# Kernel tuning notes

Measured on AMD Instinct MI355X. Metric: run time of the kernel, lower is better.

Reference implementation:

```python
import jax, jax.numpy as jnp
import numpy as np
from jax import lax

B, H, W = 32, 80, 80
K = 100                        # max_candidates
THRESH = 0.1                   # minutiae_threshold
DIST_T = 16.0
ANGLE_T = np.pi / 6.0
PI = np.pi


def _gauss_kernel1d(ks, sigma):
    c = jnp.arange(ks, dtype=jnp.float32) - ks // 2
    g = jnp.exp(-(c * c) / (2.0 * sigma * sigma))
    return g / g.sum()


def _gaussian_blur(img):  # [B,1,H,W], separable 5x5 sigma=1.5
    k = _gauss_kernel1d(5, 1.5)
    dn = ('NCHW', 'OIHW', 'NCHW')
    x = lax.conv_general_dilated(img, k.reshape(1, 1, 1, 5), (1, 1), [(0, 0), (2, 2)], dimension_numbers=dn)
    x = lax.conv_general_dilated(x, k.reshape(1, 1, 5, 1), (1, 1), [(2, 2), (0, 0)], dimension_numbers=dn)
    return x


def _up8(m):  # nearest-neighbor x8 upsample on last two dims
    return jnp.repeat(jnp.repeat(m, 8, axis=-2), 8, axis=-1)


def _detect_and_nms(score, ori, xoff, yoff):
    # score [H,W]; ori [90,H,W]; xoff/yoff [8,H,W]
    vals, idx = lax.top_k(score.reshape(-1), K)   # sorted descending == argsort by score
    valid = vals > THRESH
    rows = idx // W
    cols = idx % W
    ang_idx = jnp.argmax(ori[:, rows, cols], axis=0)   # [K]
    xo = jnp.argmax(xoff[:, rows, cols], axis=0)
    yo = jnp.argmax(yoff[:, rows, cols], axis=0)
    angles = (ang_idx.astype(jnp.float32) * 2.0 - 89.0) * (PI / 180.0)
    x = cols.astype(jnp.float32) * 8.0 + xo.astype(jnp.float32)
    y = rows.astype(jnp.float32) * 8.0 + yo.astype(jnp.float32)
    mnt = jnp.stack([x, y, angles, vals], axis=-1)     # [K,4]
    # pairwise suppression mask (cdist + circular angle delta)
    d2 = jnp.sum((mnt[:, None, :2] - mnt[None, :, :2]) ** 2, axis=-1)
    dist = jnp.sqrt(d2)
    ad = jnp.abs(angles[:, None] - angles[None, :])
    am = jnp.minimum(ad, 2.0 * PI - ad)
    sup = (dist < DIST_T) & (am < ANGLE_T)
    ar = jnp.arange(K)
    def body(i, keep):
        s = sup[i] & (ar > i)
        return jnp.where(keep[i], keep & ~s, keep)
    keep = lax.fori_loop(0, K, body, valid)
    return mnt, keep


def setup_inputs() -> dict:
    key = jax.random.key(0)
    ks = jax.random.split(key, 7)
    return {
        'segmentation': jax.random.uniform(ks[0], (B, 1, H, W), jnp.float32),
        'minutiae_score': jax.random.uniform(ks[1], (B, 1, H, W), jnp.float32),
        'minutiae_orientation': jax.random.normal(ks[2], (B, 90, H, W), jnp.float32),
        'minutiae_x_offset': jax.random.normal(ks[3], (B, 8, H, W), jnp.float32),
        'minutiae_y_offset': jax.random.normal(ks[4], (B, 8, H, W), jnp.float32),
        'orientation': jax.random.normal(ks[5], (B, 90, H, W), jnp.float32),
        'enhanced_real': jax.random.normal(ks[6], (B, 1, 8 * H, 8 * W), jnp.float32),
    }


def reference(segmentation, minutiae_score, minutiae_orientation,
              minutiae_x_offset, minutiae_y_offset, orientation, enhanced_real):
    # --- segmentation mask: round -> gaussian blur -> round
    cleaned = jnp.round(_gaussian_blur(jnp.round(segmentation[:, 0])[:, None]))[:, 0]  # [B,H,W]
    cleaned_up = _up8(cleaned)                                                          # [B,8H,8W]
    # --- minutiae detection (threshold via masked top-k) + sequential NMS
    score = minutiae_score[:, 0] * cleaned
    mnt, keep = jax.vmap(_detect_and_nms)(score, minutiae_orientation,
                                          minutiae_x_offset, minutiae_y_offset)
    # --- orientation field
    ori_idx = jnp.argmax(orientation, axis=1).astype(jnp.float32)   # [B,H,W]
    ori_field = (_up8(ori_idx) * 2.0 - 89.0) * (PI / 180.0) * cleaned_up
    # --- enhanced image: mask + per-image min-max normalize to [0,255]
    enh = enhanced_real[:, 0] * cleaned_up
    ef = enh.reshape(B, -1)
    emin = jnp.min(ef, axis=1, keepdims=True)
    emax = jnp.max(ef, axis=1, keepdims=True)
    enorm = (ef - emin) / (emax - emin + 1e-8)
    enh_visual = enorm.reshape(B, 8 * H, 8 * W) * 255.0
    return (mnt, keep.astype(jnp.float32), enh_visual, cleaned_up * 255.0, ori_field)
```

## Files before the change

### kernel.cpp

```cpp
#include <hip/hip_runtime.h>
#include <math.h>

#define BN  32
#define H   80
#define W   80
#define HW  6400
#define KC  100
#define NCH 90
#define UW  640
#define UHW 409600

static constexpr size_t OUT_MNT   = 0;
static constexpr size_t OUT_KEEP  = (size_t)BN * KC * 4;
static constexpr size_t OUT_ENH   = OUT_KEEP + (size_t)BN * KC;
static constexpr size_t OUT_CLEAN = OUT_ENH + (size_t)BN * UHW;
static constexpr size_t OUT_ORI   = OUT_CLEAN + (size_t)BN * UHW;

#define PI_F 3.14159265358979323846
#define MM_BLOCKS 64
#define ORI_MEGA  400
#define CAP 2048
#define GAT_BLOCKS 800
#define FIN_BLOCKS 12800

typedef float vfloat4 __attribute__((ext_vector_type(4)));

__device__ __forceinline__ unsigned enc_f(float f) {
    unsigned u = __float_as_uint(f);
    return (u & 0x80000000u) ? ~u : (u | 0x80000000u);
}
__device__ __forceinline__ float dec_f(unsigned k) {
    return (k & 0x80000000u) ? __uint_as_float(k ^ 0x80000000u) : __uint_as_float(~k);
}
__device__ __forceinline__ unsigned long long shflx(unsigned long long v, int off) {
    unsigned hi = (unsigned)__shfl_xor((int)(unsigned)(v >> 32), off);
    unsigned lo = (unsigned)__shfl_xor((int)(unsigned)(v & 0xffffffffull), off);
    return ((unsigned long long)hi << 32) | lo;
}

__global__ __launch_bounds__(512) void k_clean(const float* __restrict__ seg,
                                               float* __restrict__ cleaned_g) {
    __shared__ float s_in[12 * 80];
    __shared__ float s_h[12 * 80];
    const int blk = blockIdx.x;
    const int b = blk / 10, band = blk % 10;
    const int r0 = band * 8 - 2;
    const int tid = threadIdx.x;

    float g[5];
    {
        float s = 0.f;
        #pragma unroll
        for (int i = 0; i < 5; i++) {
            float c = (float)(i - 2);
            g[i] = expf(-(c * c) / 4.5f);
            s += g[i];
        }
        #pragma unroll
        for (int i = 0; i < 5; i++) g[i] /= s;
    }

    for (int i = tid; i < 12 * 80; i += 512) {
        int lr = i / 80, w = i % 80;
        int gr = r0 + lr;
        s_in[i] = (gr >= 0 && gr < H) ? rintf(seg[(size_t)b * HW + gr * W + w]) : 0.f;
    }
    __syncthreads();
    for (int i = tid; i < 12 * 80; i += 512) {
        int lr = i / 80, w = i % 80;
        float acc = 0.f;
        #pragma unroll
        for (int dx = -2; dx <= 2; dx++) {
            int ww = w + dx;
            if (ww >= 0 && ww < W) acc += s_in[lr * 80 + ww] * g[dx + 2];
        }
        s_h[i] = acc;
    }
    __syncthreads();
    for (int i = tid; i < 8 * 80; i += 512) {
        int k = i / 80, w = i % 80;
        float acc = 0.f;
        #pragma unroll
        for (int dy = 0; dy < 5; dy++) acc += s_h[(k + dy) * 80 + w] * g[dy];
        cleaned_g[(size_t)b * HW + (band * 8 + k) * W + w] = rintf(acc);
    }
}

__global__ __launch_bounds__(512) void k_mega(const float* __restrict__ mscore,
                                              const float* __restrict__ cleaned,
                                              const float* __restrict__ ori,
                                              const float* __restrict__ enh,
                                              float* __restrict__ ori_idx,
                                              float* __restrict__ pmin,
                                              float* __restrict__ pmax,
                                              int* __restrict__ ws_idx,
                                              float* __restrict__ ws_val) {
    __shared__ __align__(16) char um[20480];
    __shared__ unsigned long long s_sel[KC];
    __shared__ unsigned s_rm[HW / 32];
    __shared__ int s_cnt[5];
    __shared__ int s_n;
    __shared__ float s_T;
    __shared__ int s_mode;
    __shared__ float smin[8], smax[8];

    const int bx = blockIdx.x, tid = threadIdx.x;
    const int lane = tid & 63;

    if (bx < BN) {
        unsigned long long* s_cand = (unsigned long long*)um;
        unsigned long long* s_red  = (unsigned long long*)um + CAP;
        const int b = bx;

        if (tid < HW / 32) s_rm[tid] = 0u;
        if (tid < 5) s_cnt[tid] = 0;
        __syncthreads();

        float sc[13];
        #pragma unroll
        for (int j = 0; j < 13; j++) {
            int i = j * 512 + tid;
            sc[j] = (i < HW) ? mscore[(size_t)b * HW + i] * cleaned[(size_t)b * HW + i]
                             : -1.0f;
        }

        int c0 = 0, c1 = 0, c2 = 0, c3 = 0, c4 = 0;
        #pragma unroll
        for (int j = 0; j < 13; j++) {
            float v = sc[j];
            c0 += (v > 0.95f); c1 += (v > 0.9f); c2 += (v > 0.8f);
            c3 += (v > 0.5f);  c4 += (v > 0.0f);
        }
        #pragma unroll
        for (int off = 32; off > 0; off >>= 1) {
            c0 += __shfl_xor(c0, off); c1 += __shfl_xor(c1, off);
            c2 += __shfl_xor(c2, off); c3 += __shfl_xor(c3, off);
            c4 += __shfl_xor(c4, off);
        }
        if (lane == 0) {
            atomicAdd(&s_cnt[0], c0); atomicAdd(&s_cnt[1], c1);
            atomicAdd(&s_cnt[2], c2); atomicAdd(&s_cnt[3], c3);
            atomicAdd(&s_cnt[4], c4);
        }
        __syncthreads();

        if (tid == 0) {
            int n95 = s_cnt[0], n90 = s_cnt[1], n80 = s_cnt[2], n50 = s_cnt[3], n0 = s_cnt[4];
            int mode; float T = 0.f;
            if (n0 < KC)                      { mode = 1; }
            else if (n95 >= KC && n95 <= CAP) { mode = 0; T = 0.95f; }
            else if (n90 >= KC && n90 <= CAP) { mode = 0; T = 0.9f; }
            else if (n80 >= KC && n80 <= CAP) { mode = 0; T = 0.8f; }
            else if (n50 >= KC && n50 <= CAP) { mode = 0; T = 0.5f; }
            else if (n0 <= CAP)               { mode = 0; T = 0.0f; }
            else                              { mode = 2; }
            s_mode = mode; s_T = T; s_n = 0;
        }
        __syncthreads();
        const int mode = s_mode;

        if (mode != 2) {
            const float T = s_T;
            #pragma unroll
            for (int j = 0; j < 13; j++) {
                int i = j * 512 + tid;
                bool take = (mode == 0) ? (sc[j] > T)
                                        : (sc[j] > 0.f || (i < 256 && sc[j] == 0.0f));
                if (take) {
                    int pos = atomicAdd(&s_n, 1);
                    s_cand[pos] = ((unsigned long long)enc_f(sc[j]) << 32) | (unsigned)(HW - i);
                }
            }
            __syncthreads();
            const int n = s_n;
            for (int c = tid; c < n; c += 512) {
                unsigned long long kk = s_cand[c];
                int rank = 0;
                for (int m = 0; m < n; m++) rank += (s_cand[m] > kk) ? 1 : 0;
                if (rank < KC) s_sel[rank] = kk;
            }
            __syncthreads();
        } else {
            for (int k = 0; k < KC; k++) {
                unsigned long long lmax = 0ull;
                #pragma unroll
                for (int j = 0; j < 13; j++) {
                    int i = j * 512 + tid;
                    if (i < HW && sc[j] >= 0.f && !((s_rm[i >> 5] >> (i & 31)) & 1u)) {
                        unsigned long long kk =
                            ((unsigned long long)enc_f(sc[j]) << 32) | (unsigned)(HW - i);
                        if (kk > lmax) lmax = kk;
                    }
                }
                s_red[tid] = lmax;
                __syncthreads();
                for (int off = 256; off > 0; off >>= 1) {
                    if (tid < off) {
                        unsigned long long o = s_red[tid + off];
                        if (o > s_red[tid]) s_red[tid] = o;
                    }
                    __syncthreads();
                }
                if (tid == 0) {
                    unsigned long long wkey = s_red[0];
                    s_sel[k] = wkey;
                    int wi = HW - (int)(wkey & 0xffffffffull);
                    s_rm[wi >> 5] |= 1u << (wi & 31);
                }
                __syncthreads();
            }
        }

        if (tid < KC) {
            unsigned long long e = s_sel[tid];
            ws_idx[(size_t)b * KC + tid] = HW - (int)(e & 0xffffffffull);
            ws_val[(size_t)b * KC + tid] = dec_f((unsigned)(e >> 32));
        }
    } else if (bx < BN + ORI_MEGA) {
        float4* s_bv = (float4*)um;
        float4* s_bj = (float4*)um + 512;
        const int grp = tid >> 7, ln = tid & 127;
        const int p4 = (bx - BN) * 128 + ln;
        const int b = p4 / (HW / 4), pp = p4 % (HW / 4);
        const float4* o = (const float4*)(ori + (size_t)b * NCH * HW) + pp;
        const int cs = (grp * NCH) >> 2, ce = ((grp + 1) * NCH) >> 2;

        float4 bv = o[(size_t)cs * (HW / 4)];
        float4 bj = make_float4((float)cs, (float)cs, (float)cs, (float)cs);
        for (int j = cs + 1; j < ce; j++) {
            float4 v = o[(size_t)j * (HW / 4)];
            if (v.x > bv.x) { bv.x = v.x; bj.x = (float)j; }
            if (v.y > bv.y) { bv.y = v.y; bj.y = (float)j; }
            if (v.z > bv.z) { bv.z = v.z; bj.z = (float)j; }
            if (v.w > bv.w) { bv.w = v.w; bj.w = (float)j; }
        }
        s_bv[tid] = bv; s_bj[tid] = bj;
        __syncthreads();
        if (grp == 0) {
            #pragma unroll
            for (int g = 1; g < 4; g++) {
                float4 v = s_bv[g * 128 + ln], jx = s_bj[g * 128 + ln];
                if (v.x > bv.x) { bv.x = v.x; bj.x = jx.x; }
                if (v.y > bv.y) { bv.y = v.y; bj.y = jx.y; }
                if (v.z > bv.z) { bv.z = v.z; bj.z = jx.z; }
                if (v.w > bv.w) { bv.w = v.w; bj.w = jx.w; }
            }
            ((float4*)ori_idx)[p4] = bj;
        }
    } else {
        const int mb = bx - (BN + ORI_MEGA);
        const int b = mb >> 6, chunk = mb & 63;
        const float4* e4 = (const float4*)(enh + (size_t)b * UHW);
        const float* cb = cleaned + (size_t)b * HW;

        float vmin = INFINITY, vmax = -INFINITY;
        for (int i = chunk * 512 + tid; i < UHW / 4; i += MM_BLOCKS * 512) {
            float4 v = e4[i];
            int p = i * 4;
            int Y = p / UW, X = p % UW;
            float c = cb[(Y >> 3) * W + (X >> 3)];
            float a = v.x * c, bb = v.y * c, cc = v.z * c, dd = v.w * c;
            vmin = fminf(vmin, fminf(fminf(a, bb), fminf(cc, dd)));
            vmax = fmaxf(vmax, fmaxf(fmaxf(a, bb), fmaxf(cc, dd)));
        }
        #pragma unroll
        for (int off = 32; off > 0; off >>= 1) {
            vmin = fminf(vmin, __shfl_xor(vmin, off));
            vmax = fmaxf(vmax, __shfl_xor(vmax, off));
        }
        int wave = tid >> 6;
        if (lane == 0) { smin[wave] = vmin; smax[wave] = vmax; }
        __syncthreads();
        if (tid == 0) {
            float m0 = smin[0], m1 = smax[0];
            #pragma unroll
            for (int wv = 1; wv < 8; wv++) {
                m0 = fminf(m0, smin[wv]);
                m1 = fmaxf(m1, smax[wv]);
            }
            pmin[b * MM_BLOCKS + chunk] = m0;
            pmax[b * MM_BLOCKS + chunk] = m1;
        }
    }
}

__global__ __launch_bounds__(256) void k_fg(const float* __restrict__ enh,
                                            const float* __restrict__ cleaned,
                                            const float* __restrict__ ori_idx,
                                            const float* __restrict__ pmin,
                                            const float* __restrict__ pmax,
                                            const float* __restrict__ mori,
                                            const float* __restrict__ mxo,
                                            const float* __restrict__ myo,
                                            const int* __restrict__ ws_idx,
                                            const float* __restrict__ ws_val,
                                            float* __restrict__ out) {
    const int bx = blockIdx.x, tid = threadIdx.x;

    if (bx < GAT_BLOCKS) {
        const int lane = tid & 63;
        const int wid = bx * 4 + (tid >> 6);
        const int b = wid / KC, k = wid % KC;
        const int idx = ws_idx[(size_t)b * KC + k];

        const float* pm = mori + (size_t)b * NCH * HW + idx;
        unsigned long long kk =
            ((unsigned long long)enc_f(pm[(size_t)lane * HW]) << 32) | (unsigned)(127 - lane);
        if (lane < NCH - 64) {
            unsigned long long k1 =
                ((unsigned long long)enc_f(pm[(size_t)(64 + lane) * HW]) << 32)
                | (unsigned)(127 - (64 + lane));
            if (k1 > kk) kk = k1;
        }
        unsigned long long kx = 0ull, ky = 0ull;
        if (lane >= 32 && lane < 40)
            kx = ((unsigned long long)enc_f(mxo[((size_t)b * 8 + (lane - 32)) * HW + idx]) << 32)
                 | (unsigned)(15 - (lane - 32));
        if (lane >= 40 && lane < 48)
            ky = ((unsigned long long)enc_f(myo[((size_t)b * 8 + (lane - 40)) * HW + idx]) << 32)
                 | (unsigned)(15 - (lane - 40));

        #pragma unroll
        for (int off = 32; off > 0; off >>= 1) {
            unsigned long long o;
            o = shflx(kk, off); if (o > kk) kk = o;
            o = shflx(kx, off); if (o > kx) kx = o;
            o = shflx(ky, off); if (o > ky) ky = o;
        }

        if (lane == 0) {
            int ch = 127 - (int)(kk & 0xffffffffull);
            int xo = 15  - (int)(kx & 0xffffffffull);
            int yo = 15  - (int)(ky & 0xffffffffull);
            int r = idx / W, c = idx % W;
            float4 m;
            m.x = (float)c * 8.0f + (float)xo;
            m.y = (float)r * 8.0f + (float)yo;
            m.z = ((float)ch * 2.0f - 89.0f) * (float)(PI_F / 180.0);
            m.w = ws_val[(size_t)b * KC + k];
            ((float4*)(out + OUT_MNT))[(size_t)b * KC + k] = m;
        }
    } else {
        __shared__ float s_emin, s_emax;
        const int fb = bx - GAT_BLOCKS;
        const int b = fb / 400;
        if (tid < 64) {
            float vmin = pmin[b * MM_BLOCKS + tid];
            float vmax = pmax[b * MM_BLOCKS + tid];
            #pragma unroll
            for (int off = 32; off > 0; off >>= 1) {
                vmin = fminf(vmin, __shfl_xor(vmin, off));
                vmax = fmaxf(vmax, __shfl_xor(vmax, off));
            }
            if (tid == 0) { s_emin = vmin; s_emax = vmax; }
        }
        __syncthreads();

        int t4 = fb * 256 + tid;
        int p4 = t4 % (UHW / 4);
        int p = p4 * 4;
        int Y = p / UW, X = p % UW;
        int cidx = b * HW + (Y >> 3) * W + (X >> 3);
        float c  = cleaned[cidx];
        float oi = ori_idx[cidx];
        float emin = s_emin, emax = s_emax;
        float inv = 255.0f / (emax - emin + 1e-8f);

        float4 e = ((const float4*)enh)[t4];
        vfloat4 ev;
        ev.x = (e.x * c - emin) * inv;
        ev.y = (e.y * c - emin) * inv;
        ev.z = (e.z * c - emin) * inv;
        ev.w = (e.w * c - emin) * inv;

        float cv = c * 255.0f;
        float ov = (oi * 2.0f - 89.0f) * (float)(PI_F / 180.0) * c;
        vfloat4 cvv = {cv, cv, cv, cv};
        vfloat4 ovv = {ov, ov, ov, ov};

        __builtin_nontemporal_store(ev,  ((vfloat4*)(out + OUT_ENH))   + t4);
        __builtin_nontemporal_store(cvv, ((vfloat4*)(out + OUT_CLEAN)) + t4);
        __builtin_nontemporal_store(ovv, ((vfloat4*)(out + OUT_ORI))   + t4);
    }
}

__global__ __launch_bounds__(64) void k_nms(float* __restrict__ out) {
    const int b = blockIdx.x, l = threadIdx.x;
    const float4* mnt = (const float4*)(out + OUT_MNT) + (size_t)b * KC;
    float4 m0 = mnt[l];
    bool has1 = (l + 64) < KC;
    float4 m1 = has1 ? mnt[l + 64] : make_float4(0.f, 0.f, 0.f, -1.f);
    int keep0 = (m0.w > 0.1f) ? 1 : 0;
    int keep1 = (has1 && m1.w > 0.1f) ? 1 : 0;

    for (int i = 0; i < KC; i++) {
        bool hi = i >= 64;
        int src = i & 63;
        float xi = __shfl(hi ? m1.x : m0.x, src);
        float yi = __shfl(hi ? m1.y : m0.y, src);
        float ai = __shfl(hi ? m1.z : m0.z, src);
        int   ki = __shfl(hi ? keep1 : keep0, src);
        if (ki) {
            if (keep0 && l > i) {
                float dx = xi - m0.x, dy = yi - m0.y;
                float dist = sqrtf(dx * dx + dy * dy);
                float ad = fabsf(ai - m0.z);
                float am = fminf(ad, (float)(2.0 * PI_F) - ad);
                if (dist < 16.0f && am < (float)(PI_F / 6.0)) keep0 = 0;
            }
            if (keep1 && (l + 64) > i) {
                float dx = xi - m1.x, dy = yi - m1.y;
                float dist = sqrtf(dx * dx + dy * dy);
                float ad = fabsf(ai - m1.z);
                float am = fminf(ad, (float)(2.0 * PI_F) - ad);
                if (dist < 16.0f && am < (float)(PI_F / 6.0)) keep1 = 0;
            }
        }
    }
    out[OUT_KEEP + (size_t)b * KC + l] = (float)keep0;
    if (has1) out[OUT_KEEP + (size_t)b * KC + 64 + l] = (float)keep1;
}

extern "C" void kernel_launch(void* const* d_in, const int* in_sizes, int n_in,
                              void* d_out, int out_size, void* d_ws, size_t ws_size,
                              hipStream_t stream) {
    const float* seg    = (const float*)d_in[0];
    const float* mscore = (const float*)d_in[1];
    const float* mori   = (const float*)d_in[2];
    const float* mxo    = (const float*)d_in[3];
    const float* myo    = (const float*)d_in[4];
    const float* ori    = (const float*)d_in[5];
    const float* enh    = (const float*)d_in[6];
    float* out = (float*)d_out;

    float* cleaned = (float*)d_ws;
    float* ori_idx = cleaned + (size_t)BN * HW;
    float* pmin    = ori_idx + (size_t)BN * HW;
    float* pmax    = pmin + (size_t)BN * MM_BLOCKS;
    int*   ws_idx  = (int*)(pmax + (size_t)BN * MM_BLOCKS);
    float* ws_val  = (float*)(ws_idx + (size_t)BN * KC);

    const int nMega = BN + ORI_MEGA + BN * MM_BLOCKS;
    const int nFG   = GAT_BLOCKS + FIN_BLOCKS;

    k_clean<<<BN * 10, 512, 0, stream>>>(seg, cleaned);
    k_mega<<<nMega, 512, 0, stream>>>(mscore, cleaned, ori, enh,
                                      ori_idx, pmin, pmax, ws_idx, ws_val);
    k_fg<<<nFG, 256, 0, stream>>>(enh, cleaned, ori_idx, pmin, pmax,
                                  mori, mxo, myo, ws_idx, ws_val, out);
    k_nms<<<BN, 64, 0, stream>>>(out);
}
```

Before: 95.15 us.

## Regroup kernels: merge clean with ori-argmax, fold NMS into per-batch gather block

The orientation argmax moves from the mega kernel into the pre-kernel alongside the segmentation blur, so it overlaps with the blur and leaves the mid kernel with only top-k and min/max. The separate NMS launch is removed: one block per batch now gathers all 100 candidates through shared memory and runs the suppression loop in-block. The finalize path uses 512-thread blocks, each handling four float4 per thread. This saves one launch and shortens the critical path, but the gather now uses only 32 blocks, which serialises 13 rounds per batch, and that could lengthen the tail.

```diff
diff --git a/kernel.cpp b/kernel.cpp
--- a/kernel.cpp
+++ b/kernel.cpp
@@ -18,10 +18,11 @@
 
 #define PI_F 3.14159265358979323846
 #define MM_BLOCKS 64
-#define ORI_MEGA  400
 #define CAP 2048
-#define GAT_BLOCKS 800
-#define FIN_BLOCKS 12800
+#define CLEAN_BLOCKS 320
+#define ORI_BLOCKS2 400
+#define GATHER_BLOCKS 32
+#define FIN_BLOCKS 1600
 
 typedef float vfloat4 __attribute__((ext_vector_type(4)));
 
@@ -38,63 +39,97 @@
     return ((unsigned long long)hi << 32) | lo;
 }
 
-__global__ __launch_bounds__(512) void k_clean(const float* __restrict__ seg,
-                                               float* __restrict__ cleaned_g) {
-    __shared__ float s_in[12 * 80];
-    __shared__ float s_h[12 * 80];
-    const int blk = blockIdx.x;
-    const int b = blk / 10, band = blk % 10;
-    const int r0 = band * 8 - 2;
-    const int tid = threadIdx.x;
-
-    float g[5];
-    {
-        float s = 0.f;
-        #pragma unroll
-        for (int i = 0; i < 5; i++) {
-            float c = (float)(i - 2);
-            g[i] = expf(-(c * c) / 4.5f);
-            s += g[i];
-        }
-        #pragma unroll
-        for (int i = 0; i < 5; i++) g[i] /= s;
+__global__ __launch_bounds__(512) void k_pre(const float* __restrict__ seg,
+                                             const float* __restrict__ ori,
+                                             float* __restrict__ cleaned_g,
+                                             float* __restrict__ ori_idx) {
+    __shared__ __align__(16) char um[16384];
+    const int bx = blockIdx.x, tid = threadIdx.x;
+
+    if (bx < CLEAN_BLOCKS) {
+        float* s_in = (float*)um;
+        float* s_h  = (float*)um + 960;
+        const int b = bx / 10, band = bx % 10;
+        const int r0 = band * 8 - 2;
+
+        float g[5];
+        {
+            float s = 0.f;
+            #pragma unroll
+            for (int i = 0; i < 5; i++) {
+                float c = (float)(i - 2);
+                g[i] = expf(-(c * c) / 4.5f);
+                s += g[i];
+            }
+            #pragma unroll
+            for (int i = 0; i < 5; i++) g[i] /= s;
+        }
+
+        for (int i = tid; i < 12 * 80; i += 512) {
+            int lr = i / 80, w = i % 80;
+            int gr = r0 + lr;
+            s_in[i] = (gr >= 0 && gr < H) ? rintf(seg[(size_t)b * HW + gr * W + w]) : 0.f;
+        }
+        __syncthreads();
+        for (int i = tid; i < 12 * 80; i += 512) {
+            int lr = i / 80, w = i % 80;
+            float acc = 0.f;
+            #pragma unroll
+            for (int dx = -2; dx <= 2; dx++) {
+                int ww = w + dx;
+                if (ww >= 0 && ww < W) acc += s_in[lr * 80 + ww] * g[dx + 2];
+            }
+            s_h[i] = acc;
+        }
+        __syncthreads();
+        for (int i = tid; i < 8 * 80; i += 512) {
+            int k = i / 80, w = i % 80;
+            float acc = 0.f;
+            #pragma unroll
+            for (int dy = 0; dy < 5; dy++) acc += s_h[(k + dy) * 80 + w] * g[dy];
+            cleaned_g[(size_t)b * HW + (band * 8 + k) * W + w] = rintf(acc);
+        }
+    } else {
+        float4* s_bv = (float4*)um;
+        float4* s_bj = (float4*)um + 512;
+        const int grp = tid >> 7, ln = tid & 127;
+        const int p4 = (bx - CLEAN_BLOCKS) * 128 + ln;
+        const int b = p4 / (HW / 4), pp = p4 % (HW / 4);
+        const float4* o = (const float4*)(ori + (size_t)b * NCH * HW) + pp;
+        const int cs = (grp * NCH) >> 2, ce = ((grp + 1) * NCH) >> 2;
+
+        float4 bv = o[(size_t)cs * (HW / 4)];
+        float4 bj = make_float4((float)cs, (float)cs, (float)cs, (float)cs);
+        for (int j = cs + 1; j < ce; j++) {
+            float4 v = o[(size_t)j * (HW / 4)];
+            if (v.x > bv.x) { bv.x = v.x; bj.x = (float)j; }
+            if (v.y > bv.y) { bv.y = v.y; bj.y = (float)j; }
+            if (v.z > bv.z) { bv.z = v.z; bj.z = (float)j; }
+            if (v.w > bv.w) { bv.w = v.w; bj.w = (float)j; }
+        }
+        s_bv[tid] = bv; s_bj[tid] = bj;
+        __syncthreads();
+        if (grp == 0) {
+            #pragma unroll
+            for (int g = 1; g < 4; g++) {
+                float4 v = s_bv[g * 128 + ln], jx = s_bj[g * 128 + ln];
+                if (v.x > bv.x) { bv.x = v.x; bj.x = jx.x; }
+                if (v.y > bv.y) { bv.y = v.y; bj.y = jx.y; }
+                if (v.z > bv.z) { bv.z = v.z; bj.z = jx.z; }
+                if (v.w > bv.w) { bv.w = v.w; bj.w = jx.w; }
+            }
+            ((float4*)ori_idx)[p4] = bj;
+        }
     }
-
-    for (int i = tid; i < 12 * 80; i += 512) {
-        int lr = i / 80, w = i % 80;
-        int gr = r0 + lr;
-        s_in[i] = (gr >= 0 && gr < H) ? rintf(seg[(size_t)b * HW + gr * W + w]) : 0.f;
-    }
-    __syncthreads();
-    for (int i = tid; i < 12 * 80; i += 512) {
-        int lr = i / 80, w = i % 80;
-        float acc = 0.f;
-        #pragma unroll
-        for (int dx = -2; dx <= 2; dx++) {
-            int ww = w + dx;
-            if (ww >= 0 && ww < W) acc += s_in[lr * 80 + ww] * g[dx + 2];
-        }
-        s_h[i] = acc;
-    }
-    __syncthreads();
-    for (int i = tid; i < 8 * 80; i += 512) {
-        int k = i / 80, w = i % 80;
-        float acc = 0.f;
-        #pragma unroll
-        for (int dy = 0; dy < 5; dy++) acc += s_h[(k + dy) * 80 + w] * g[dy];
-        cleaned_g[(size_t)b * HW + (band * 8 + k) * W + w] = rintf(acc);
-    }
-}
-
-__global__ __launch_bounds__(512) void k_mega(const float* __restrict__ mscore,
-                                              const float* __restrict__ cleaned,
-                                              const float* __restrict__ ori,
-                                              const float* __restrict__ enh,
-                                              float* __restrict__ ori_idx,
-                                              float* __restrict__ pmin,
-                                              float* __restrict__ pmax,
-                                              int* __restrict__ ws_idx,
-                                              float* __restrict__ ws_val) {
+}
+
+__global__ __launch_bounds__(512) void k_mid(const float* __restrict__ mscore,
+                                             const float* __restrict__ cleaned,
+                                             const float* __restrict__ enh,
+                                             float* __restrict__ pmin,
+                                             float* __restrict__ pmax,
+                                             int* __restrict__ ws_idx,
+                                             float* __restrict__ ws_val) {
     __shared__ __align__(16) char um[20480];
     __shared__ unsigned long long s_sel[KC];
     __shared__ unsigned s_rm[HW / 32];
@@ -216,39 +251,8 @@
             ws_idx[(size_t)b * KC + tid] = HW - (int)(e & 0xffffffffull);
             ws_val[(size_t)b * KC + tid] = dec_f((unsigned)(e >> 32));
         }
-    } else if (bx < BN + ORI_MEGA) {
-        float4* s_bv = (float4*)um;
-        float4* s_bj = (float4*)um + 512;
-        const int grp = tid >> 7, ln = tid & 127;
-        const int p4 = (bx - BN) * 128 + ln;
-        const int b = p4 / (HW / 4), pp = p4 % (HW / 4);
-        const float4* o = (const float4*)(ori + (size_t)b * NCH * HW) + pp;
-        const int cs = (grp * NCH) >> 2, ce = ((grp + 1) * NCH) >> 2;
-
-        float4 bv = o[(size_t)cs * (HW / 4)];
-        float4 bj = make_float4((float)cs, (float)cs, (float)cs, (float)cs);
-        for (int j = cs + 1; j < ce; j++) {
-            float4 v = o[(size_t)j * (HW / 4)];
-            if (v.x > bv.x) { bv.x = v.x; bj.x = (float)j; }
-            if (v.y > bv.y) { bv.y = v.y; bj.y = (float)j; }
-            if (v.z > bv.z) { bv.z = v.z; bj.z = (float)j; }
-            if (v.w > bv.w) { bv.w = v.w; bj.w = (float)j; }
-        }
-        s_bv[tid] = bv; s_bj[tid] = bj;
-        __syncthreads();
-        if (grp == 0) {
-            #pragma unroll
-            for (int g = 1; g < 4; g++) {
-                float4 v = s_bv[g * 128 + ln], jx = s_bj[g * 128 + ln];
-                if (v.x > bv.x) { bv.x = v.x; bj.x = jx.x; }
-                if (v.y > bv.y) { bv.y = v.y; bj.y = jx.y; }
-                if (v.z > bv.z) { bv.z = v.z; bj.z = jx.z; }
-                if (v.w > bv.w) { bv.w = v.w; bj.w = jx.w; }
-            }
-            ((float4*)ori_idx)[p4] = bj;
-        }
     } else {
-        const int mb = bx - (BN + ORI_MEGA);
+        const int mb = bx - BN;
         const int b = mb >> 6, chunk = mb & 63;
         const float4* e4 = (const float4*)(enh + (size_t)b * UHW);
         const float* cb = cleaned + (size_t)b * HW;
@@ -284,7 +288,7 @@
     }
 }
 
-__global__ __launch_bounds__(256) void k_fg(const float* __restrict__ enh,
+__global__ __launch_bounds__(512) void k_fg(const float* __restrict__ enh,
                                             const float* __restrict__ cleaned,
                                             const float* __restrict__ ori_idx,
                                             const float* __restrict__ pmin,
@@ -297,53 +301,99 @@
                                             float* __restrict__ out) {
     const int bx = blockIdx.x, tid = threadIdx.x;
 
-    if (bx < GAT_BLOCKS) {
-        const int lane = tid & 63;
-        const int wid = bx * 4 + (tid >> 6);
-        const int b = wid / KC, k = wid % KC;
-        const int idx = ws_idx[(size_t)b * KC + k];
-
-        const float* pm = mori + (size_t)b * NCH * HW + idx;
-        unsigned long long kk =
-            ((unsigned long long)enc_f(pm[(size_t)lane * HW]) << 32) | (unsigned)(127 - lane);
-        if (lane < NCH - 64) {
-            unsigned long long k1 =
-                ((unsigned long long)enc_f(pm[(size_t)(64 + lane) * HW]) << 32)
-                | (unsigned)(127 - (64 + lane));
-            if (k1 > kk) kk = k1;
-        }
-        unsigned long long kx = 0ull, ky = 0ull;
-        if (lane >= 32 && lane < 40)
-            kx = ((unsigned long long)enc_f(mxo[((size_t)b * 8 + (lane - 32)) * HW + idx]) << 32)
-                 | (unsigned)(15 - (lane - 32));
-        if (lane >= 40 && lane < 48)
-            ky = ((unsigned long long)enc_f(myo[((size_t)b * 8 + (lane - 40)) * HW + idx]) << 32)
-                 | (unsigned)(15 - (lane - 40));
-
-        #pragma unroll
-        for (int off = 32; off > 0; off >>= 1) {
-            unsigned long long o;
-            o = shflx(kk, off); if (o > kk) kk = o;
-            o = shflx(kx, off); if (o > kx) kx = o;
-            o = shflx(ky, off); if (o > ky) ky = o;
-        }
-
-        if (lane == 0) {
-            int ch = 127 - (int)(kk & 0xffffffffull);
-            int xo = 15  - (int)(kx & 0xffffffffull);
-            int yo = 15  - (int)(ky & 0xffffffffull);
-            int r = idx / W, c = idx % W;
-            float4 m;
-            m.x = (float)c * 8.0f + (float)xo;
-            m.y = (float)r * 8.0f + (float)yo;
-            m.z = ((float)ch * 2.0f - 89.0f) * (float)(PI_F / 180.0);
-            m.w = ws_val[(size_t)b * KC + k];
-            ((float4*)(out + OUT_MNT))[(size_t)b * KC + k] = m;
+    if (bx < GATHER_BLOCKS) {
+        __shared__ float s_mx[KC], s_my[KC], s_ma[KC], s_mv[KC];
+        const int b = bx;
+        const int wave = tid >> 6, lane = tid & 63;
+
+        for (int r = 0; r < 13; r++) {
+            const int k = r * 8 + wave;
+            if (k < KC) {
+                const int idx = ws_idx[(size_t)b * KC + k];
+                const float* pm = mori + (size_t)b * NCH * HW + idx;
+                unsigned long long kk =
+                    ((unsigned long long)enc_f(pm[(size_t)lane * HW]) << 32) | (unsigned)(127 - lane);
+                if (lane < NCH - 64) {
+                    unsigned long long k1 =
+                        ((unsigned long long)enc_f(pm[(size_t)(64 + lane) * HW]) << 32)
+                        | (unsigned)(127 - (64 + lane));
+                    if (k1 > kk) kk = k1;
+                }
+                unsigned long long kx = 0ull, ky = 0ull;
+                if (lane >= 32 && lane < 40)
+                    kx = ((unsigned long long)enc_f(mxo[((size_t)b * 8 + (lane - 32)) * HW + idx]) << 32)
+                         | (unsigned)(15 - (lane - 32));
+                if (lane >= 40 && lane < 48)
+                    ky = ((unsigned long long)enc_f(myo[((size_t)b * 8 + (lane - 40)) * HW + idx]) << 32)
+                         | (unsigned)(15 - (lane - 40));
+
+                #pragma unroll
+                for (int off = 32; off > 0; off >>= 1) {
+                    unsigned long long o;
+                    o = shflx(kk, off); if (o > kk) kk = o;
+                    o = shflx(kx, off); if (o > kx) kx = o;
+                    o = shflx(ky, off); if (o > ky) ky = o;
+                }
+
+                if (lane == 0) {
+                    int ch = 127 - (int)(kk & 0xffffffffull);
+                    int xo = 15  - (int)(kx & 0xffffffffull);
+                    int yo = 15  - (int)(ky & 0xffffffffull);
+                    int rr = idx / W, cc = idx % W;
+                    float4 m;
+                    m.x = (float)cc * 8.0f + (float)xo;
+                    m.y = (float)rr * 8.0f + (float)yo;
+                    m.z = ((float)ch * 2.0f - 89.0f) * (float)(PI_F / 180.0);
+                    m.w = ws_val[(size_t)b * KC + k];
+                    ((float4*)(out + OUT_MNT))[(size_t)b * KC + k] = m;
+                    s_mx[k] = m.x; s_my[k] = m.y; s_ma[k] = m.z; s_mv[k] = m.w;
+                }
+            }
+        }
+        __syncthreads();
+
+        if (tid < 64) {
+            const int l = tid;
+            float x0 = s_mx[l], y0 = s_my[l], a0 = s_ma[l], v0 = s_mv[l];
+            bool has1 = (l + 64) < KC;
+            float x1 = has1 ? s_mx[l + 64] : 0.f;
+            float y1 = has1 ? s_my[l + 64] : 0.f;
+            float a1 = has1 ? s_ma[l + 64] : 0.f;
+            float v1 = has1 ? s_mv[l + 64] : -1.f;
+            int keep0 = (v0 > 0.1f) ? 1 : 0;
+            int keep1 = (has1 && v1 > 0.1f) ? 1 : 0;
+
+            for (int i = 0; i < KC; i++) {
+                bool hi = i >= 64;
+                int src = i & 63;
+                float xi = __shfl(hi ? x1 : x0, src);
+                float yi = __shfl(hi ? y1 : y0, src);
+                float ai = __shfl(hi ? a1 : a0, src);
+                int   ki = __shfl(hi ? keep1 : keep0, src);
+                if (ki) {
+                    if (keep0 && l > i) {
+                        float dx = xi - x0, dy = yi - y0;
+                        float dist = sqrtf(dx * dx + dy * dy);
+                        float ad = fabsf(ai - a0);
+                        float am = fminf(ad, (float)(2.0 * PI_F) - ad);
+                        if (dist < 16.0f && am < (float)(PI_F / 6.0)) keep0 = 0;
+                    }
+                    if (keep1 && (l + 64) > i) {
+                        float dx = xi - x1, dy = yi - y1;
+                        float dist = sqrtf(dx * dx + dy * dy);
+                        float ad = fabsf(ai - a1);
+                        float am = fminf(ad, (float)(2.0 * PI_F) - ad);
+                        if (dist < 16.0f && am < (float)(PI_F / 6.0)) keep1 = 0;
+                    }
+                }
+            }
+            out[OUT_KEEP + (size_t)b * KC + l] = (float)keep0;
+            if (has1) out[OUT_KEEP + (size_t)b * KC + 64 + l] = (float)keep1;
         }
     } else {
         __shared__ float s_emin, s_emax;
-        const int fb = bx - GAT_BLOCKS;
-        const int b = fb / 400;
+        const int fb = bx - GATHER_BLOCKS;
+        const int b = fb / 50, chunk = fb % 50;
         if (tid < 64) {
             float vmin = pmin[b * MM_BLOCKS + tid];
             float vmax = pmax[b * MM_BLOCKS + tid];
@@ -355,70 +405,37 @@
             if (tid == 0) { s_emin = vmin; s_emax = vmax; }
         }
         __syncthreads();
-
-        int t4 = fb * 256 + tid;
-        int p4 = t4 % (UHW / 4);
-        int p = p4 * 4;
-        int Y = p / UW, X = p % UW;
-        int cidx = b * HW + (Y >> 3) * W + (X >> 3);
-        float c  = cleaned[cidx];
-        float oi = ori_idx[cidx];
-        float emin = s_emin, emax = s_emax;
-        float inv = 255.0f / (emax - emin + 1e-8f);
-
-        float4 e = ((const float4*)enh)[t4];
-        vfloat4 ev;
-        ev.x = (e.x * c - emin) * inv;
-        ev.y = (e.y * c - emin) * inv;
-        ev.z = (e.z * c - emin) * inv;
-        ev.w = (e.w * c - emin) * inv;
-
-        float cv = c * 255.0f;
-        float ov = (oi * 2.0f - 89.0f) * (float)(PI_F / 180.0) * c;
-        vfloat4 cvv = {cv, cv, cv, cv};
-        vfloat4 ovv = {ov, ov, ov, ov};
-
-        __builtin_nontemporal_store(ev,  ((vfloat4*)(out + OUT_ENH))   + t4);
-        __builtin_nontemporal_store(cvv, ((vfloat4*)(out + OUT_CLEAN)) + t4);
-        __builtin_nontemporal_store(ovv, ((vfloat4*)(out + OUT_ORI))   + t4);
+        const float emin = s_emin, emax = s_emax;
+        const float inv = 255.0f / (emax - emin + 1e-8f);
+        const float4* e4 = (const float4*)(enh + (size_t)b * UHW);
+        const float* cb = cleaned + (size_t)b * HW;
+        const float* ob = ori_idx + (size_t)b * HW;
+        const int base = chunk * 2048;
+
+        #pragma unroll
+        for (int it = 0; it < 4; it++) {
+            const int i = base + it * 512 + tid;
+            float4 e = e4[i];
+            int p = i * 4;
+            int Y = p / UW, X = p % UW;
+            int cidx = (Y >> 3) * W + (X >> 3);
+            float c  = cb[cidx];
+            float oi = ob[cidx];
+            vfloat4 ev;
+            ev.x = (e.x * c - emin) * inv;
+            ev.y = (e.y * c - emin) * inv;
+            ev.z = (e.z * c - emin) * inv;
+            ev.w = (e.w * c - emin) * inv;
+            float cv = c * 255.0f;
+            float ov = (oi * 2.0f - 89.0f) * (float)(PI_F / 180.0) * c;
+            vfloat4 cvv = {cv, cv, cv, cv};
+            vfloat4 ovv = {ov, ov, ov, ov};
+            size_t t4 = (size_t)b * (UHW / 4) + i;
+            __builtin_nontemporal_store(ev,  ((vfloat4*)(out + OUT_ENH))   + t4);
+            __builtin_nontemporal_store(cvv, ((vfloat4*)(out + OUT_CLEAN)) + t4);
+            __builtin_nontemporal_store(ovv, ((vfloat4*)(out + OUT_ORI))   + t4);
+        }
     }
-}
-
-__global__ __launch_bounds__(64) void k_nms(float* __restrict__ out) {
-    const int b = blockIdx.x, l = threadIdx.x;
-    const float4* mnt = (const float4*)(out + OUT_MNT) + (size_t)b * KC;
-    float4 m0 = mnt[l];
-    bool has1 = (l + 64) < KC;
-    float4 m1 = has1 ? mnt[l + 64] : make_float4(0.f, 0.f, 0.f, -1.f);
-    int keep0 = (m0.w > 0.1f) ? 1 : 0;
-    int keep1 = (has1 && m1.w > 0.1f) ? 1 : 0;
-
-    for (int i = 0; i < KC; i++) {
-        bool hi = i >= 64;
-        int src = i & 63;
-        float xi = __shfl(hi ? m1.x : m0.x, src);
-        float yi = __shfl(hi ? m1.y : m0.y, src);
-        float ai = __shfl(hi ? m1.z : m0.z, src);
-        int   ki = __shfl(hi ? keep1 : keep0, src);
-        if (ki) {
-            if (keep0 && l > i) {
-                float dx = xi - m0.x, dy = yi - m0.y;
-                float dist = sqrtf(dx * dx + dy * dy);
-                float ad = fabsf(ai - m0.z);
-                float am = fminf(ad, (float)(2.0 * PI_F) - ad);
-                if (dist < 16.0f && am < (float)(PI_F / 6.0)) keep0 = 0;
-            }
-            if (keep1 && (l + 64) > i) {
-                float dx = xi - m1.x, dy = yi - m1.y;
-                float dist = sqrtf(dx * dx + dy * dy);
-                float ad = fabsf(ai - m1.z);
-                float am = fminf(ad, (float)(2.0 * PI_F) - ad);
-                if (dist < 16.0f && am < (float)(PI_F / 6.0)) keep1 = 0;
-            }
-        }
-    }
-    out[OUT_KEEP + (size_t)b * KC + l] = (float)keep0;
-    if (has1) out[OUT_KEEP + (size_t)b * KC + 64 + l] = (float)keep1;
 }
 
 extern "C" void kernel_launch(void* const* d_in, const int* in_sizes, int n_in,
@@ -440,13 +457,12 @@
     int*   ws_idx  = (int*)(pmax + (size_t)BN * MM_BLOCKS);
     float* ws_val  = (float*)(ws_idx + (size_t)BN * KC);
 
-    const int nMega = BN + ORI_MEGA + BN * MM_BLOCKS;
-    const int nFG   = GAT_BLOCKS + FIN_BLOCKS;
-
-    k_clean<<<BN * 10, 512, 0, stream>>>(seg, cleaned);
-    k_mega<<<nMega, 512, 0, stream>>>(mscore, cleaned, ori, enh,
-                                      ori_idx, pmin, pmax, ws_idx, ws_val);
-    k_fg<<<nFG, 256, 0, stream>>>(enh, cleaned, ori_idx, pmin, pmax,
+    const int nPre = CLEAN_BLOCKS + ORI_BLOCKS2;
+    const int nMid = BN + BN * MM_BLOCKS;
+    const int nFG  = GATHER_BLOCKS + FIN_BLOCKS;
+
+    k_pre<<<nPre, 512, 0, stream>>>(seg, ori, cleaned, ori_idx);
+    k_mid<<<nMid, 512, 0, stream>>>(mscore, cleaned, enh, pmin, pmax, ws_idx, ws_val);
+    k_fg<<<nFG, 512, 0, stream>>>(enh, cleaned, ori_idx, pmin, pmax,
                                   mori, mxo, myo, ws_idx, ws_val, out);
-    k_nms<<<BN, 64, 0, stream>>>(out);
-}
+}
```

Result: slower. 110.1 us (+15.7%).

## Move orientation argmax into the blur kernel to rebalance stage work

Applied to the files above, without the earlier changes.

The orientation argmax blocks move out of the mega kernel into the segmentation-blur kernel, since they do not depend on the cleaned mask. The first kernel then runs blur and argmax side by side, and the middle kernel keeps only top-k and min/max. The aim is to overlap the large orientation read with the small, latency-bound blur stage and to shorten the critical middle stage. The first kernel now has more work and a larger shared footprint, and the top-k blocks still define how long the middle stage takes.

```diff
diff --git a/kernel.cpp b/kernel.cpp
--- a/kernel.cpp
+++ b/kernel.cpp
@@ -18,8 +18,9 @@
 
 #define PI_F 3.14159265358979323846
 #define MM_BLOCKS 64
-#define ORI_MEGA  400
 #define CAP 2048
+#define CLEAN_BLOCKS 320
+#define ORI_BLOCKS2 400
 #define GAT_BLOCKS 800
 #define FIN_BLOCKS 12800
 
@@ -38,63 +39,97 @@
     return ((unsigned long long)hi << 32) | lo;
 }
 
-__global__ __launch_bounds__(512) void k_clean(const float* __restrict__ seg,
-                                               float* __restrict__ cleaned_g) {
-    __shared__ float s_in[12 * 80];
-    __shared__ float s_h[12 * 80];
-    const int blk = blockIdx.x;
-    const int b = blk / 10, band = blk % 10;
-    const int r0 = band * 8 - 2;
-    const int tid = threadIdx.x;
-
-    float g[5];
-    {
-        float s = 0.f;
-        #pragma unroll
-        for (int i = 0; i < 5; i++) {
-            float c = (float)(i - 2);
-            g[i] = expf(-(c * c) / 4.5f);
-            s += g[i];
-        }
-        #pragma unroll
-        for (int i = 0; i < 5; i++) g[i] /= s;
+__global__ __launch_bounds__(512) void k_pre(const float* __restrict__ seg,
+                                             const float* __restrict__ ori,
+                                             float* __restrict__ cleaned_g,
+                                             float* __restrict__ ori_idx) {
+    __shared__ __align__(16) char um[16384];
+    const int bx = blockIdx.x, tid = threadIdx.x;
+
+    if (bx < CLEAN_BLOCKS) {
+        float* s_in = (float*)um;
+        float* s_h  = (float*)um + 960;
+        const int b = bx / 10, band = bx % 10;
+        const int r0 = band * 8 - 2;
+
+        float g[5];
+        {
+            float s = 0.f;
+            #pragma unroll
+            for (int i = 0; i < 5; i++) {
+                float c = (float)(i - 2);
+                g[i] = expf(-(c * c) / 4.5f);
+                s += g[i];
+            }
+            #pragma unroll
+            for (int i = 0; i < 5; i++) g[i] /= s;
+        }
+
+        for (int i = tid; i < 12 * 80; i += 512) {
+            int lr = i / 80, w = i % 80;
+            int gr = r0 + lr;
+            s_in[i] = (gr >= 0 && gr < H) ? rintf(seg[(size_t)b * HW + gr * W + w]) : 0.f;
+        }
+        __syncthreads();
+        for (int i = tid; i < 12 * 80; i += 512) {
+            int lr = i / 80, w = i % 80;
+            float acc = 0.f;
+            #pragma unroll
+            for (int dx = -2; dx <= 2; dx++) {
+                int ww = w + dx;
+                if (ww >= 0 && ww < W) acc += s_in[lr * 80 + ww] * g[dx + 2];
+            }
+            s_h[i] = acc;
+        }
+        __syncthreads();
+        for (int i = tid; i < 8 * 80; i += 512) {
+            int k = i / 80, w = i % 80;
+            float acc = 0.f;
+            #pragma unroll
+            for (int dy = 0; dy < 5; dy++) acc += s_h[(k + dy) * 80 + w] * g[dy];
+            cleaned_g[(size_t)b * HW + (band * 8 + k) * W + w] = rintf(acc);
+        }
+    } else {
+        float4* s_bv = (float4*)um;
+        float4* s_bj = (float4*)um + 512;
+        const int grp = tid >> 7, ln = tid & 127;
+        const int p4 = (bx - CLEAN_BLOCKS) * 128 + ln;
+        const int b = p4 / (HW / 4), pp = p4 % (HW / 4);
+        const float4* o = (const float4*)(ori + (size_t)b * NCH * HW) + pp;
+        const int cs = (grp * NCH) >> 2, ce = ((grp + 1) * NCH) >> 2;
+
+        float4 bv = o[(size_t)cs * (HW / 4)];
+        float4 bj = make_float4((float)cs, (float)cs, (float)cs, (float)cs);
+        for (int j = cs + 1; j < ce; j++) {
+            float4 v = o[(size_t)j * (HW / 4)];
+            if (v.x > bv.x) { bv.x = v.x; bj.x = (float)j; }
+            if (v.y > bv.y) { bv.y = v.y; bj.y = (float)j; }
+            if (v.z > bv.z) { bv.z = v.z; bj.z = (float)j; }
+            if (v.w > bv.w) { bv.w = v.w; bj.w = (float)j; }
+        }
+        s_bv[tid] = bv; s_bj[tid] = bj;
+        __syncthreads();
+        if (grp == 0) {
+            #pragma unroll
+            for (int g = 1; g < 4; g++) {
+                float4 v = s_bv[g * 128 + ln], jx = s_bj[g * 128 + ln];
+                if (v.x > bv.x) { bv.x = v.x; bj.x = jx.x; }
+                if (v.y > bv.y) { bv.y = v.y; bj.y = jx.y; }
+                if (v.z > bv.z) { bv.z = v.z; bj.z = jx.z; }
+                if (v.w > bv.w) { bv.w = v.w; bj.w = jx.w; }
+            }
+            ((float4*)ori_idx)[p4] = bj;
+        }
     }
-
-    for (int i = tid; i < 12 * 80; i += 512) {
-        int lr = i / 80, w = i % 80;
-        int gr = r0 + lr;
-        s_in[i] = (gr >= 0 && gr < H) ? rintf(seg[(size_t)b * HW + gr * W + w]) : 0.f;
-    }
-    __syncthreads();
-    for (int i = tid; i < 12 * 80; i += 512) {
-        int lr = i / 80, w = i % 80;
-        float acc = 0.f;
-        #pragma unroll
-        for (int dx = -2; dx <= 2; dx++) {
-            int ww = w + dx;
-            if (ww >= 0 && ww < W) acc += s_in[lr * 80 + ww] * g[dx + 2];
-        }
-        s_h[i] = acc;
-    }
-    __syncthreads();
-    for (int i = tid; i < 8 * 80; i += 512) {
-        int k = i / 80, w = i % 80;
-        float acc = 0.f;
-        #pragma unroll
-        for (int dy = 0; dy < 5; dy++) acc += s_h[(k + dy) * 80 + w] * g[dy];
-        cleaned_g[(size_t)b * HW + (band * 8 + k) * W + w] = rintf(acc);
-    }
-}
-
-__global__ __launch_bounds__(512) void k_mega(const float* __restrict__ mscore,
-                                              const float* __restrict__ cleaned,
-                                              const float* __restrict__ ori,
-                                              const float* __restrict__ enh,
-                                              float* __restrict__ ori_idx,
-                                              float* __restrict__ pmin,
-                                              float* __restrict__ pmax,
-                                              int* __restrict__ ws_idx,
-                                              float* __restrict__ ws_val) {
+}
+
+__global__ __launch_bounds__(512) void k_mid(const float* __restrict__ mscore,
+                                             const float* __restrict__ cleaned,
+                                             const float* __restrict__ enh,
+                                             float* __restrict__ pmin,
+                                             float* __restrict__ pmax,
+                                             int* __restrict__ ws_idx,
+                                             float* __restrict__ ws_val) {
     __shared__ __align__(16) char um[20480];
     __shared__ unsigned long long s_sel[KC];
     __shared__ unsigned s_rm[HW / 32];
@@ -216,39 +251,8 @@
             ws_idx[(size_t)b * KC + tid] = HW - (int)(e & 0xffffffffull);
             ws_val[(size_t)b * KC + tid] = dec_f((unsigned)(e >> 32));
         }
-    } else if (bx < BN + ORI_MEGA) {
-        float4* s_bv = (float4*)um;
-        float4* s_bj = (float4*)um + 512;
-        const int grp = tid >> 7, ln = tid & 127;
-        const int p4 = (bx - BN) * 128 + ln;
-        const int b = p4 / (HW / 4), pp = p4 % (HW / 4);
-        const float4* o = (const float4*)(ori + (size_t)b * NCH * HW) + pp;
-        const int cs = (grp * NCH) >> 2, ce = ((grp + 1) * NCH) >> 2;
-
-        float4 bv = o[(size_t)cs * (HW / 4)];
-        float4 bj = make_float4((float)cs, (float)cs, (float)cs, (float)cs);
-        for (int j = cs + 1; j < ce; j++) {
-            float4 v = o[(size_t)j * (HW / 4)];
-            if (v.x > bv.x) { bv.x = v.x; bj.x = (float)j; }
-            if (v.y > bv.y) { bv.y = v.y; bj.y = (float)j; }
-            if (v.z > bv.z) { bv.z = v.z; bj.z = (float)j; }
-            if (v.w > bv.w) { bv.w = v.w; bj.w = (float)j; }
-        }
-        s_bv[tid] = bv; s_bj[tid] = bj;
-        __syncthreads();
-        if (grp == 0) {
-            #pragma unroll
-            for (int g = 1; g < 4; g++) {
-                float4 v = s_bv[g * 128 + ln], jx = s_bj[g * 128 + ln];
-                if (v.x > bv.x) { bv.x = v.x; bj.x = jx.x; }
-                if (v.y > bv.y) { bv.y = v.y; bj.y = jx.y; }
-                if (v.z > bv.z) { bv.z = v.z; bj.z = jx.z; }
-                if (v.w > bv.w) { bv.w = v.w; bj.w = jx.w; }
-            }
-            ((float4*)ori_idx)[p4] = bj;
-        }
     } else {
-        const int mb = bx - (BN + ORI_MEGA);
+        const int mb = bx - BN;
         const int b = mb >> 6, chunk = mb & 63;
         const float4* e4 = (const float4*)(enh + (size_t)b * UHW);
         const float* cb = cleaned + (size_t)b * HW;
@@ -440,12 +444,12 @@
     int*   ws_idx  = (int*)(pmax + (size_t)BN * MM_BLOCKS);
     float* ws_val  = (float*)(ws_idx + (size_t)BN * KC);
 
-    const int nMega = BN + ORI_MEGA + BN * MM_BLOCKS;
-    const int nFG   = GAT_BLOCKS + FIN_BLOCKS;
-
-    k_clean<<<BN * 10, 512, 0, stream>>>(seg, cleaned);
-    k_mega<<<nMega, 512, 0, stream>>>(mscore, cleaned, ori, enh,
-                                      ori_idx, pmin, pmax, ws_idx, ws_val);
+    const int nPre = CLEAN_BLOCKS + ORI_BLOCKS2;
+    const int nMid = BN + BN * MM_BLOCKS;
+    const int nFG  = GAT_BLOCKS + FIN_BLOCKS;
+
+    k_pre<<<nPre, 512, 0, stream>>>(seg, ori, cleaned, ori_idx);
+    k_mid<<<nMid, 512, 0, stream>>>(mscore, cleaned, enh, pmin, pmax, ws_idx, ws_val);
     k_fg<<<nFG, 256, 0, stream>>>(enh, cleaned, ori_idx, pmin, pmax,
                                   mori, mxo, myo, ws_idx, ws_val, out);
     k_nms<<<BN, 64, 0, stream>>>(out);
```

Result: no change. 94.07 us (-1.1%).
